# Optimization experiments

Measured on AMD Instinct MI355X. Metric: run time of the kernel, lower is better.

## Reference

```python
import jax, jax.numpy as jnp
import numpy as np

B_SZ, SEQ, D_IN = 8, 4096, 1024
STATE, HEADS = 1024, 16
HEAD_DIM = STATE // HEADS
LN_EPS = 1e-5


def setup_inputs() -> dict:
    key = jax.random.key(0)
    ks = jax.random.split(key, 10)
    inp = {
        "x": jax.random.normal(ks[0], (B_SZ, SEQ, D_IN), dtype=jnp.float32),
        "W_in": jax.random.normal(ks[1], (STATE, D_IN), dtype=jnp.float32) * (1.0 / np.sqrt(D_IN)),
        "b_in": jnp.zeros((STATE,), dtype=jnp.float32),
        "log_A": jax.random.normal(ks[2], (HEADS, HEAD_DIM), dtype=jnp.float32) * 0.1 + 0.1,
        "B_p": jax.random.normal(ks[3], (HEADS, HEAD_DIM), dtype=jnp.float32) * 0.1 + 0.1,
        "C_p": jax.random.normal(ks[4], (HEADS, HEAD_DIM), dtype=jnp.float32) * 0.1 + 0.1,
        "W_out": jax.random.normal(ks[5], (STATE, STATE), dtype=jnp.float32) * (1.0 / np.sqrt(STATE)),
        "b_out": jnp.zeros((STATE,), dtype=jnp.float32),
        "gamma": jnp.ones((STATE,), dtype=jnp.float32),
        "beta": jnp.zeros((STATE,), dtype=jnp.float32),
    }
    return inp


def reference(x, W_in, b_in, log_A, B_p, C_p, W_out, b_out, gamma, beta):
    Bsz, S, _ = x.shape
    H, Dh = log_A.shape
    # input projection: (B,S,state)
    h = jnp.einsum("bsd,ed->bse", x, W_in) + b_in
    h = h.reshape(Bsz, S, H, Dh)
    decay = jnp.exp(-jax.nn.softplus(log_A))  # (H,Dh), time-invariant

    def step(s, xt):  # s,xt: (B,H,Dh)
        s = s * decay + B_p * xt
        return s, C_p * s

    s0 = jnp.zeros((Bsz, H, Dh), dtype=h.dtype)
    _, ys = jax.lax.scan(step, s0, jnp.swapaxes(h, 0, 1))  # ys: (S,B,H,Dh)
    y = jnp.swapaxes(ys, 0, 1).reshape(Bsz, S, H * Dh)
    out = jnp.einsum("bse,fe->bsf", y, W_out) + b_out
    # dropout in eval mode = identity; layer norm over last dim
    mu = out.mean(-1, keepdims=True)
    var = out.var(-1, keepdims=True)
    return (out - mu) * jax.lax.rsqrt(var + LN_EPS) * gamma + beta
```

## Files before the change

### kernel.cpp

```cpp
#include <hip/hip_runtime.h>

#define B_SZ  8
#define SEQ   4096
#define D_IN  1024
#define STATE 1024
#define M_TOT (B_SZ * SEQ)
#define LN_EPS 1e-5f
#define GK    1024
#define GN    1024

#define SCAN_L 256
#define SCAN_W 64

typedef short short8_t __attribute__((ext_vector_type(8)));
typedef float f32x4 __attribute__((ext_vector_type(4)));

__device__ __forceinline__ unsigned short f2bf(float f) {
  union { float f; unsigned u; } v; v.f = f;
  unsigned r = v.u + 0x7fffu + ((v.u >> 16) & 1u);
  return (unsigned short)(r >> 16);
}
__device__ __forceinline__ float bf2f(unsigned short h) {
  union { unsigned u; float f; } v; v.u = ((unsigned)h) << 16;
  return v.f;
}

__device__ __forceinline__ void gload16(const void* g, void* l) {
  __builtin_amdgcn_global_load_lds(
      (const __attribute__((address_space(1))) void*)g,
      (__attribute__((address_space(3))) void*)l, 16, 0, 0);
}

#define FENCE()  asm volatile("" ::: "memory")
#define BAR()    __builtin_amdgcn_s_barrier()
#define SCHED0() __builtin_amdgcn_sched_barrier(0)

__device__ __forceinline__ void glue_pre_mfma() { FENCE(); BAR(); }
__device__ __forceinline__ void close_phase()   { SCHED0(); FENCE(); BAR(); SCHED0(); }

__global__ __launch_bounds__(256) void cast_kernel(const float* __restrict__ in,
                                                   unsigned short* __restrict__ out,
                                                   int n4) {
  int i = blockIdx.x * 256 + threadIdx.x;
  if (i < n4) {
    float4 v = ((const float4*)in)[i];
    ushort4 o;
    o.x = f2bf(v.x); o.y = f2bf(v.y); o.z = f2bf(v.z); o.w = f2bf(v.w);
    ((ushort4*)out)[i] = o;
  }
}


__device__ __forceinline__ void stage(const char* gbase, char* dbase, int t, int q) {
  gload16(gbase + (q * 131072 + t * 128), dbase + q * 8192);
}

template <int H, int NH, bool RDA, bool RDB>
__device__ __forceinline__ void phase_reads(const char* pAk0, const char* pAk1,
                                            const char* pBk0, const char* pBk1,
                                            short8_t (&a)[4][2], short8_t (&b)[2][2]) {
  if (RDB) {
#pragma unroll
    for (int nf = 0; nf < 2; nf++)
      b[nf][0] = *(const short8_t*)(pBk0 + ((NH * 32 + nf * 16) << 7));
  }
  if (RDA) {
#pragma unroll
    for (int mf = 0; mf < 4; mf++)
      a[mf][0] = *(const short8_t*)(pAk0 + ((H * 64 + mf * 16) << 7));
  }
  if (RDB) {
#pragma unroll
    for (int nf = 0; nf < 2; nf++)
      b[nf][1] = *(const short8_t*)(pBk1 + ((NH * 32 + nf * 16) << 7));
  }
  if (RDA) {
#pragma unroll
    for (int mf = 0; mf < 4; mf++)
      a[mf][1] = *(const short8_t*)(pAk1 + ((H * 64 + mf * 16) << 7));
  }
}

template <int H, int NH>
__device__ __forceinline__ void phase_mfma(short8_t (&a)[4][2], short8_t (&b)[2][2],
                                           f32x4 (&acc)[8][4]) {
  __builtin_amdgcn_s_setprio(1);
#pragma unroll
  for (int ks = 0; ks < 2; ks++)
#pragma unroll
    for (int mf = 0; mf < 4; mf++)
#pragma unroll
      for (int nf = 0; nf < 2; nf++)
        acc[H * 4 + mf][NH * 2 + nf] = __builtin_amdgcn_mfma_f32_16x16x32_bf16(
            a[mf][ks], b[nf][ks], acc[H * 4 + mf][NH * 2 + nf], 0, 0, 0);
  __builtin_amdgcn_s_setprio(0);
}

__global__ __launch_bounds__(512, 2) void gemm256(
    const unsigned short* __restrict__ A,
    const unsigned short* __restrict__ Bt,
    const float* __restrict__ bias,
    unsigned short* __restrict__ C,
    int M) {
  __shared__ __attribute__((aligned(16))) unsigned short As[2][256 * 64];
  __shared__ __attribute__((aligned(16))) unsigned short Bs[2][256 * 64];

  const int tid = threadIdx.x;
  const int w = tid >> 6, lane = tid & 63;
  const int wm = w >> 2, wn = w & 3;
  const int fr = lane & 15;
  const int fkb = (lane >> 4) * 16;

  const int nwg = gridDim.x;
  const int cpx = nwg >> 3;
  const int bid = blockIdx.x;
  const int wg = (bid & 7) * cpx + (bid >> 3);
  const int nbx = GN >> 8;
  const long m0 = (long)(wg / nbx) * 256;
  const long n0 = (long)(wg % nbx) * 256;

  const int xorv = (fr & 7) << 4;
  const int lo0 = (fr * 128 + 0  + fkb) ^ xorv;
  const int lo1 = (fr * 128 + 64 + fkb) ^ xorv;
  const char* pA0k0 = (const char*)&As[0][0] + wm * 16384 + lo0;
  const char* pA0k1 = (const char*)&As[0][0] + wm * 16384 + lo1;
  const char* pA1k0 = (const char*)&As[1][0] + wm * 16384 + lo0;
  const char* pA1k1 = (const char*)&As[1][0] + wm * 16384 + lo1;
  const char* pB0k0 = (const char*)&Bs[0][0] + wn * 8192 + lo0;
  const char* pB0k1 = (const char*)&Bs[0][0] + wn * 8192 + lo1;
  const char* pB1k0 = (const char*)&Bs[1][0] + wn * 8192 + lo0;
  const char* pB1k1 = (const char*)&Bs[1][0] + wn * 8192 + lo1;

  const int srow = tid >> 3;
  const int c2 = ((tid & 7) * 16) ^ ((srow & 7) << 4);
  const char* gA0 = (const char*)(A  + (m0 + srow) * (long)GK) + c2;
  const char* gB0 = (const char*)(Bt + (n0 + srow) * (long)GK) + c2;
  char* dA0 = (char*)&As[0][0] + ((tid >> 6) << 10);
  char* dA1 = (char*)&As[1][0] + ((tid >> 6) << 10);
  char* dB0 = (char*)&Bs[0][0] + ((tid >> 6) << 10);
  char* dB1 = (char*)&Bs[1][0] + ((tid >> 6) << 10);

  short8_t a[4][2], b[2][2];
  f32x4 acc[8][4] = {};

  const int nit = (GK >> 6) >> 1;

#pragma unroll
  for (int q = 0; q < 4; q++) stage(gA0, dA0, 0, q);
#pragma unroll
  for (int q = 0; q < 4; q++) stage(gB0, dB0, 0, q);
  stage(gA0, dA1, 1, 0);
  stage(gA0, dA1, 1, 2);
  asm volatile("s_waitcnt vmcnt(2)" ::: "memory");
  FENCE(); BAR(); SCHED0();

#pragma unroll 1
  for (int i = 0; i < nit; ++i) {
    const bool last = (i == nit - 1);
    const int t1 = 2 * i + 1, t2 = 2 * i + 2, t3 = 2 * i + 3;

    phase_reads<0, 0, true, true>(pA0k0, pA0k1, pB0k0, pB0k1, a, b);
    stage(gA0, dA1, t1, 1);
    stage(gA0, dA1, t1, 3);
    glue_pre_mfma();
    phase_mfma<0, 0>(a, b, acc);
    close_phase();

    phase_reads<0, 1, false, true>(pA0k0, pA0k1, pB0k0, pB0k1, a, b);
    stage(gB0, dB1, t1, 0);
    stage(gB0, dB1, t1, 1);
    glue_pre_mfma();
    phase_mfma<0, 1>(a, b, acc);
    close_phase();

    phase_reads<1, 1, true, false>(pA0k0, pA0k1, pB0k0, pB0k1, a, b);
    stage(gB0, dB1, t1, 2);
    stage(gB0, dB1, t1, 3);
    if (!last) {
      stage(gA0, dA0, t2, 0);
      stage(gA0, dA0, t2, 2);
    }
    glue_pre_mfma();
    phase_mfma<1, 1>(a, b, acc);
    close_phase();

    phase_reads<1, 0, false, true>(pA0k0, pA0k1, pB0k0, pB0k1, a, b);
    glue_pre_mfma();
    phase_mfma<1, 0>(a, b, acc);
    if (last) { asm volatile("s_waitcnt vmcnt(0)" ::: "memory"); }
    else      { asm volatile("s_waitcnt vmcnt(2)" ::: "memory"); }
    close_phase();

    phase_reads<0, 0, true, true>(pA1k0, pA1k1, pB1k0, pB1k1, a, b);
    if (!last) {
      stage(gA0, dA0, t2, 1);
      stage(gA0, dA0, t2, 3);
    }
    glue_pre_mfma();
    phase_mfma<0, 0>(a, b, acc);
    close_phase();

    phase_reads<0, 1, false, true>(pA1k0, pA1k1, pB1k0, pB1k1, a, b);
    if (!last) {
      stage(gB0, dB0, t2, 0);
      stage(gB0, dB0, t2, 1);
    }
    glue_pre_mfma();
    phase_mfma<0, 1>(a, b, acc);
    close_phase();

    phase_reads<1, 1, true, false>(pA1k0, pA1k1, pB1k0, pB1k1, a, b);
    if (!last) {
      stage(gB0, dB0, t2, 2);
      stage(gB0, dB0, t2, 3);
    }
    glue_pre_mfma();
    phase_mfma<1, 1>(a, b, acc);
    close_phase();

    phase_reads<1, 0, false, true>(pA1k0, pA1k1, pB1k0, pB1k1, a, b);
    if (!last) {
      stage(gA0, dA1, t3, 0);
      stage(gA0, dA1, t3, 2);
    }
    glue_pre_mfma();
    phase_mfma<1, 0>(a, b, acc);
    if (!last) { asm volatile("s_waitcnt vmcnt(2)" ::: "memory"); }
    close_phase();
  }

  const int cc = lane & 15;
  const int cr = (lane >> 4) * 4;
#pragma unroll
  for (int nf = 0; nf < 4; nf++) {
    const long col = n0 + wn * 64 + nf * 16 + cc;
    const float bv = bias[col];
#pragma unroll
    for (int mf = 0; mf < 8; mf++) {
#pragma unroll
      for (int r = 0; r < 4; r++) {
        const long row = m0 + wm * 128 + mf * 16 + cr + r;
        C[row * (long)GN + col] = f2bf(acc[mf][nf][r] + bv);
      }
    }
  }
}

__global__ __launch_bounds__(256) void scan_kernel(
    const unsigned short* __restrict__ h,
    const float* __restrict__ log_A,
    const float* __restrict__ Bp,
    const float* __restrict__ Cp,
    unsigned short* __restrict__ y) {
  const int e = blockIdx.x * 256 + threadIdx.x;
  const int chunk = blockIdx.y;
  const int b = blockIdx.z;
  const float la = log_A[e];
  const float d = expf(-log1pf(expf(la)));
  const float bp = Bp[e];
  const float cp = Cp[e];
  const long base = ((long)b * SEQ) * STATE + e;
  const int t0 = chunk * SCAN_L;
  const int tw = (t0 >= SCAN_W) ? (t0 - SCAN_W) : 0;
  float s = 0.f;
  for (int t = tw; t < t0; ++t)
    s = fmaf(s, d, bp * bf2f(h[base + (long)t * STATE]));
  for (int t = t0; t < t0 + SCAN_L; ++t) {
    s = fmaf(s, d, bp * bf2f(h[base + (long)t * STATE]));
    y[base + (long)t * STATE] = f2bf(cp * s);
  }
}

__global__ __launch_bounds__(256) void ln_kernel(
    const unsigned short* __restrict__ X,
    const float* __restrict__ gamma,
    const float* __restrict__ beta,
    float* __restrict__ out) {
  const int row = blockIdx.x;
  const int tid = threadIdx.x;
  const long base = (long)row * STATE;
  ushort4 v = *(const ushort4*)&X[base + tid * 4];
  float x0 = bf2f(v.x), x1 = bf2f(v.y), x2 = bf2f(v.z), x3 = bf2f(v.w);
  float s = x0 + x1 + x2 + x3;
  float q = x0 * x0 + x1 * x1 + x2 * x2 + x3 * x3;
#pragma unroll
  for (int o = 32; o > 0; o >>= 1) {
    s += __shfl_xor(s, o);
    q += __shfl_xor(q, o);
  }
  __shared__ float sw[4], qw[4];
  const int wave = tid >> 6, lane = tid & 63;
  if (lane == 0) { sw[wave] = s; qw[wave] = q; }
  __syncthreads();
  s = sw[0] + sw[1] + sw[2] + sw[3];
  q = qw[0] + qw[1] + qw[2] + qw[3];
  const float mu = s * (1.0f / STATE);
  const float var = q * (1.0f / STATE) - mu * mu;
  const float inv = rsqrtf(var + LN_EPS);
  const int c = tid * 4;
  float4 o;
  o.x = (x0 - mu) * inv * gamma[c + 0] + beta[c + 0];
  o.y = (x1 - mu) * inv * gamma[c + 1] + beta[c + 1];
  o.z = (x2 - mu) * inv * gamma[c + 2] + beta[c + 2];
  o.w = (x3 - mu) * inv * gamma[c + 3] + beta[c + 3];
  *(float4*)&out[base + tid * 4] = o;
}

extern "C" void kernel_launch(void* const* d_in, const int* in_sizes, int n_in,
                              void* d_out, int out_size, void* d_ws, size_t ws_size,
                              hipStream_t stream) {
  const float* x     = (const float*)d_in[0];
  const float* W_in  = (const float*)d_in[1];
  const float* b_in  = (const float*)d_in[2];
  const float* log_A = (const float*)d_in[3];
  const float* Bp    = (const float*)d_in[4];
  const float* Cp    = (const float*)d_in[5];
  const float* W_out = (const float*)d_in[6];
  const float* b_out = (const float*)d_in[7];
  const float* gamma = (const float*)d_in[8];
  const float* beta  = (const float*)d_in[9];
  float* out = (float*)d_out;

  char* ws = (char*)d_ws;
  unsigned short* Wi_b = (unsigned short*)(ws);
  unsigned short* Wo_b = (unsigned short*)(ws + (2ull << 20));
  unsigned short* xb   = (unsigned short*)(ws + (4ull << 20));
  unsigned short* hb   = (unsigned short*)(ws + (68ull << 20));

  cast_kernel<<<(M_TOT * D_IN / 4) / 256, 256, 0, stream>>>(x, xb, M_TOT * D_IN / 4);
  cast_kernel<<<(STATE * D_IN / 4) / 256, 256, 0, stream>>>(W_in, Wi_b, STATE * D_IN / 4);
  cast_kernel<<<(STATE * STATE / 4) / 256, 256, 0, stream>>>(W_out, Wo_b, STATE * STATE / 4);

  gemm256<<<dim3((GN / 256) * (M_TOT / 256)), 512, 0, stream>>>(
      xb, Wi_b, b_in, hb, M_TOT);

  scan_kernel<<<dim3(STATE / 256, SEQ / SCAN_L, B_SZ), 256, 0, stream>>>(
      hb, log_A, Bp, Cp, xb);

  gemm256<<<dim3((GN / 256) * (M_TOT / 256)), 512, 0, stream>>>(
      xb, Wo_b, b_out, hb, M_TOT);

  ln_kernel<<<M_TOT, 256, 0, stream>>>(hb, gamma, beta, out);
}
```

Before: 297.1 us.

## Simplify GEMM prefetch to whole-tile stages, stage epilogue via LDS, halve scan chunk

Three separate changes. The GEMM main loop drops its interleaved quarter-tile prefetch spread across phases and instead issues the full next A/B tile at the start of each half-iteration, waiting for all loads to finish (vmcnt(0)). The epilogue now writes bf16 results into swizzled LDS and reads them back as 16-byte rows for coalesced global stores, in place of scattered 2-byte stores. The scan chunk length is halved, which gives more parallel chunks but more carry-propagation work and more passes over the chunk boundaries. Fully draining the load queue each half-iteration may cost some load/compute overlap.

After: 274.0 us. 7.8% less time.

```diff
diff --git a/kernel.cpp b/kernel.cpp
--- a/kernel.cpp
+++ b/kernel.cpp
@@ -9,7 +9,7 @@
 #define GK    1024
 #define GN    1024
 
-#define SCAN_L 256
+#define SCAN_L 128
 #define SCAN_W 64
 
 typedef short short8_t __attribute__((ext_vector_type(8)));
@@ -149,37 +149,29 @@
   for (int q = 0; q < 4; q++) stage(gA0, dA0, 0, q);
 #pragma unroll
   for (int q = 0; q < 4; q++) stage(gB0, dB0, 0, q);
-  stage(gA0, dA1, 1, 0);
-  stage(gA0, dA1, 1, 2);
-  asm volatile("s_waitcnt vmcnt(2)" ::: "memory");
+  asm volatile("s_waitcnt vmcnt(0)" ::: "memory");
   FENCE(); BAR(); SCHED0();
 
 #pragma unroll 1
   for (int i = 0; i < nit; ++i) {
     const bool last = (i == nit - 1);
-    const int t1 = 2 * i + 1, t2 = 2 * i + 2, t3 = 2 * i + 3;
+    const int t1 = 2 * i + 1, t2 = 2 * i + 2;
 
     phase_reads<0, 0, true, true>(pA0k0, pA0k1, pB0k0, pB0k1, a, b);
-    stage(gA0, dA1, t1, 1);
-    stage(gA0, dA1, t1, 3);
+#pragma unroll
+    for (int q = 0; q < 4; q++) stage(gA0, dA1, t1, q);
+#pragma unroll
+    for (int q = 0; q < 4; q++) stage(gB0, dB1, t1, q);
     glue_pre_mfma();
     phase_mfma<0, 0>(a, b, acc);
     close_phase();
 
     phase_reads<0, 1, false, true>(pA0k0, pA0k1, pB0k0, pB0k1, a, b);
-    stage(gB0, dB1, t1, 0);
-    stage(gB0, dB1, t1, 1);
     glue_pre_mfma();
     phase_mfma<0, 1>(a, b, acc);
     close_phase();
 
     phase_reads<1, 1, true, false>(pA0k0, pA0k1, pB0k0, pB0k1, a, b);
-    stage(gB0, dB1, t1, 2);
-    stage(gB0, dB1, t1, 3);
-    if (!last) {
-      stage(gA0, dA0, t2, 0);
-      stage(gA0, dA0, t2, 2);
-    }
     glue_pre_mfma();
     phase_mfma<1, 1>(a, b, acc);
     close_phase();
@@ -187,62 +179,64 @@
     phase_reads<1, 0, false, true>(pA0k0, pA0k1, pB0k0, pB0k1, a, b);
     glue_pre_mfma();
     phase_mfma<1, 0>(a, b, acc);
-    if (last) { asm volatile("s_waitcnt vmcnt(0)" ::: "memory"); }
-    else      { asm volatile("s_waitcnt vmcnt(2)" ::: "memory"); }
+    asm volatile("s_waitcnt vmcnt(0)" ::: "memory");
     close_phase();
 
     phase_reads<0, 0, true, true>(pA1k0, pA1k1, pB1k0, pB1k1, a, b);
     if (!last) {
-      stage(gA0, dA0, t2, 1);
-      stage(gA0, dA0, t2, 3);
+#pragma unroll
+      for (int q = 0; q < 4; q++) stage(gA0, dA0, t2, q);
+#pragma unroll
+      for (int q = 0; q < 4; q++) stage(gB0, dB0, t2, q);
     }
     glue_pre_mfma();
     phase_mfma<0, 0>(a, b, acc);
     close_phase();
 
     phase_reads<0, 1, false, true>(pA1k0, pA1k1, pB1k0, pB1k1, a, b);
-    if (!last) {
-      stage(gB0, dB0, t2, 0);
-      stage(gB0, dB0, t2, 1);
-    }
     glue_pre_mfma();
     phase_mfma<0, 1>(a, b, acc);
     close_phase();
 
     phase_reads<1, 1, true, false>(pA1k0, pA1k1, pB1k0, pB1k1, a, b);
-    if (!last) {
-      stage(gB0, dB0, t2, 2);
-      stage(gB0, dB0, t2, 3);
-    }
     glue_pre_mfma();
     phase_mfma<1, 1>(a, b, acc);
     close_phase();
 
     phase_reads<1, 0, false, true>(pA1k0, pA1k1, pB1k0, pB1k1, a, b);
-    if (!last) {
-      stage(gA0, dA1, t3, 0);
-      stage(gA0, dA1, t3, 2);
-    }
     glue_pre_mfma();
     phase_mfma<1, 0>(a, b, acc);
-    if (!last) { asm volatile("s_waitcnt vmcnt(2)" ::: "memory"); }
+    if (!last) { asm volatile("s_waitcnt vmcnt(0)" ::: "memory"); }
     close_phase();
   }
 
   const int cc = lane & 15;
   const int cr = (lane >> 4) * 4;
-#pragma unroll
-  for (int nf = 0; nf < 4; nf++) {
-    const long col = n0 + wn * 64 + nf * 16 + cc;
-    const float bv = bias[col];
-#pragma unroll
-    for (int mf = 0; mf < 8; mf++) {
-#pragma unroll
-      for (int r = 0; r < 4; r++) {
-        const long row = m0 + wm * 128 + mf * 16 + cr + r;
-        C[row * (long)GN + col] = f2bf(acc[mf][nf][r] + bv);
+  char* epi = (w < 4) ? ((char*)&As[0][0] + w * 16384)
+                      : ((char*)&Bs[0][0] + (w - 4) * 16384);
+  float bv[4];
+#pragma unroll
+  for (int nf = 0; nf < 4; nf++) bv[nf] = bias[n0 + wn * 64 + nf * 16 + cc];
+#pragma unroll
+  for (int mf = 0; mf < 8; mf++) {
+#pragma unroll
+    for (int r = 0; r < 4; r++) {
+      const int row = mf * 16 + cr + r;
+      const int rx = (row & 7) << 4;
+#pragma unroll
+      for (int nf = 0; nf < 4; nf++) {
+        const int off = (row * 128 + (nf * 16 + cc) * 2) ^ rx;
+        *(unsigned short*)(epi + off) = f2bf(acc[mf][nf][r] + bv[nf]);
       }
     }
+  }
+  const int rr = lane >> 3;
+  const int rdoff = (lane * 16) ^ ((rr & 7) << 4);
+  char* cbase = (char*)C + (m0 + wm * 128) * (GN * 2) + n0 * 2 + wn * 128 + (lane & 7) * 16;
+#pragma unroll
+  for (int s = 0; s < 16; s++) {
+    short8_t vv = *(const short8_t*)(epi + s * 1024 + rdoff);
+    *(short8_t*)(cbase + (long)(s * 8 + rr) * (GN * 2)) = vv;
   }
 }
 
```
